# Kernel tuning notes

Hardware: AMD Instinct MI355X
Metric: run time of the kernel (lower is better)

## Reference

```python
import jax, jax.numpy as jnp
import numpy as np


def setup_inputs() -> dict:
    key = jax.random.key(0)
    k1, k2, k3, k4 = jax.random.split(key, 4)
    B, C, N, T = 16, 64, 2048, 24
    x = jax.random.normal(k1, (B, C, N, T), dtype=jnp.float32)
    adj = jax.random.uniform(k2, (N, N), dtype=jnp.float32)
    # Learned parameters (initialized to zeros in the original; random here
    # so the reference exercises nontrivial math).
    Gw = jax.random.normal(k3, (T, T), dtype=jnp.float32) * 0.1
    alpha = jax.random.normal(k4, (C,), dtype=jnp.float32) * 0.1
    return {"x": x, "adj": adj, "Gw": Gw, "alpha": alpha}


def reference(x, adj, Gw, alpha):
    # k = q = einsum('bcnt,c->bnt')  (channel-reduced features)
    k = jnp.einsum('bcnt,c->bnt', x, alpha)
    # scores[b,n,m] = k[b,n,:] @ Gw @ k[b,m,:]
    kG = jnp.einsum('bnt,ts->bns', k, Gw)          # [B,N,T]
    scores = jnp.einsum('bns,bms->bnm', kG, k)     # [B,N,N]
    att = jax.nn.softmax(scores, axis=-1)
    # adjacency-masked weighted aggregation over neighbors
    return jnp.einsum('bnm,bcmt->bcnt', att * adj, x)
```

## Files before the change

kernel.cpp:

```cpp
#include <hip/hip_runtime.h>
#include <hip/hip_bf16.h>

#define BB 16
#define CC 64
#define NN 2048
#define TT 24
#define JJ (CC*TT)
#define NT (NN*TT)

typedef unsigned short u16;
typedef unsigned int u32;
typedef __bf16 bf16x8 __attribute__((ext_vector_type(8)));
typedef u16 u16x8 __attribute__((ext_vector_type(8)));
typedef float f32x4 __attribute__((ext_vector_type(4)));
typedef u32 u32x4 __attribute__((ext_vector_type(4)));

static __device__ __forceinline__ u16 f2bf(float f) {
  union { float f; u32 u; } v; v.f = f;
  u32 u = v.u;
  u += 0x7fffu + ((u >> 16) & 1u);
  return (u16)(u >> 16);
}
static __device__ __forceinline__ float bf2f(u16 h) {
  union { u32 u; float f; } v; v.u = ((u32)h) << 16; return v.f;
}
static __device__ __forceinline__ bf16x8 ld_bf8(const u16* p) {
  return __builtin_bit_cast(bf16x8, *(const u16x8*)p);
}
#define MFMA16(a,b,c) __builtin_amdgcn_mfma_f32_16x16x32_bf16((a),(b),(c),0,0,0)

static __device__ __forceinline__ void gload16(const u16* g, u16* lds) {
  __builtin_amdgcn_global_load_lds(
      (const __attribute__((address_space(1))) u32*)g,
      (__attribute__((address_space(3))) u32*)lds, 16, 0, 0);
}
static __device__ __forceinline__ int SG(int r) { return (r ^ (r >> 2)) & 3; }

__global__ __launch_bounds__(256) void kA(
    const float* __restrict__ x, const float* __restrict__ alpha,
    u16* __restrict__ xT, float* __restrict__ kpart) {
  int bid = blockIdx.x;
  int b  = bid >> 5;
  int mt = (bid >> 1) & 15;
  int ch = bid & 1;
  int m0 = mt * 128;
  int tid = threadIdx.x;
  __shared__ float tile[128][25];
  float kacc[12];
  #pragma unroll
  for (int e = 0; e < 12; ++e) kacc[e] = 0.f;

  for (int c = ch*32; c < ch*32 + 32; ++c) {
    const float4* src4 = (const float4*)(x + ((size_t)(b*CC + c)*NN + m0)*TT);
    float a = alpha[c];
    float4 v[3];
    #pragma unroll
    for (int q = 0; q < 3; ++q) v[q] = src4[tid*3 + q];
    __syncthreads();
    #pragma unroll
    for (int q = 0; q < 3; ++q) {
      int idx = tid*3 + q;
      int mm = idx / 6, off = (idx - mm*6)*4;
      tile[mm][off]   = v[q].x; tile[mm][off+1] = v[q].y;
      tile[mm][off+2] = v[q].z; tile[mm][off+3] = v[q].w;
      kacc[q*4+0] += a*v[q].x; kacc[q*4+1] += a*v[q].y;
      kacc[q*4+2] += a*v[q].z; kacc[q*4+3] += a*v[q].w;
    }
    __syncthreads();
    #pragma unroll
    for (int qq = 0; qq < 6; ++qq) {
      int idx = tid*6 + qq;
      int t = idx >> 6, mp = idx & 63;
      u32 lo = f2bf(tile[2*mp][t]);
      u32 hi = f2bf(tile[2*mp+1][t]);
      ((u32*)(xT + ((size_t)((b*CC + c)*TT + t))*NN + m0))[mp] = lo | (hi << 16);
    }
  }
  float* kp = kpart + (size_t)ch*BB*NT + (size_t)b*NT + (size_t)m0*TT + tid*12;
  #pragma unroll
  for (int q = 0; q < 3; ++q)
    *(float4*)(kp + q*4) = make_float4(kacc[q*4], kacc[q*4+1], kacc[q*4+2], kacc[q*4+3]);
}

__global__ __launch_bounds__(256) void k2_prep(
    const float* __restrict__ kpart, const float* __restrict__ Gw,
    u16* __restrict__ kGhi, u16* __restrict__ kGlo,
    u16* __restrict__ kPhi, u16* __restrict__ kPlo) {
  __shared__ float gw[TT*TT];
  for (int i = threadIdx.x; i < TT*TT; i += 256) gw[i] = Gw[i];
  __syncthreads();
  int row = blockIdx.x * blockDim.x + threadIdx.x;
  if (row >= BB*NN) return;
  float kr[TT];
  const float4* s0 = (const float4*)(kpart + (size_t)row*TT);
  const float4* s1 = (const float4*)(kpart + (size_t)BB*NT + (size_t)row*TT);
  #pragma unroll
  for (int q = 0; q < 6; ++q) {
    float4 a = s0[q], bv = s1[q];
    kr[4*q]   = a.x + bv.x; kr[4*q+1] = a.y + bv.y;
    kr[4*q+2] = a.z + bv.z; kr[4*q+3] = a.w + bv.w;
  }
  float o[TT];
  #pragma unroll
  for (int s = 0; s < TT; ++s) o[s] = 0.f;
  #pragma unroll
  for (int t = 0; t < TT; ++t) {
    float kv = kr[t];
    #pragma unroll
    for (int s = 0; s < TT; ++s) o[s] += kv * gw[t*TT + s];
  }
  size_t rb = (size_t)row * 32;
  u32* ghi = (u32*)(kGhi + rb); u32* glo = (u32*)(kGlo + rb);
  u32* phi = (u32*)(kPhi + rb); u32* plo = (u32*)(kPlo + rb);
  #pragma unroll
  for (int sp = 0; sp < 16; ++sp) {
    float v0 = (2*sp   < TT) ? o[2*sp]   : 0.f;
    float v1 = (2*sp+1 < TT) ? o[2*sp+1] : 0.f;
    u16 h0 = f2bf(v0), h1 = f2bf(v1);
    u16 l0 = f2bf(v0 - bf2f(h0)), l1 = f2bf(v1 - bf2f(h1));
    ghi[sp] = (u32)h0 | ((u32)h1 << 16);
    glo[sp] = (u32)l0 | ((u32)l1 << 16);
    float w0 = (2*sp   < TT) ? kr[2*sp]   : 0.f;
    float w1 = (2*sp+1 < TT) ? kr[2*sp+1] : 0.f;
    u16 ph0 = f2bf(w0), ph1 = f2bf(w1);
    u16 pl0 = f2bf(w0 - bf2f(ph0)), pl1 = f2bf(w1 - bf2f(ph1));
    phi[sp] = (u32)ph0 | ((u32)ph1 << 16);
    plo[sp] = (u32)pl0 | ((u32)pl1 << 16);
  }
}

__global__ __launch_bounds__(256) void kW(
    const u16* __restrict__ kGhi, const u16* __restrict__ kGlo,
    const u16* __restrict__ kPhi, const u16* __restrict__ kPlo,
    const float* __restrict__ adj, u16* __restrict__ Wm,
    float* __restrict__ Zpart) {
  int bid = blockIdx.x;
  int b = bid >> 8, nt = (bid >> 4) & 15, mt = bid & 15;
  int tid = threadIdx.x;
  int w = tid >> 6, l = tid & 63;
  __shared__ u16 wlds[128][128];
  size_t kgb = ((size_t)b*NN + nt*128) * 32;
  bf16x8 ahi[2], alo[2];
  #pragma unroll
  for (int nf = 0; nf < 2; ++nf) {
    size_t off = kgb + (size_t)(w*32 + nf*16 + (l & 15))*32 + (l >> 4)*8;
    ahi[nf] = ld_bf8(kGhi + off);
    alo[nf] = ld_bf8(kGlo + off);
  }
  f32x4 acc[2][8];
  #pragma unroll
  for (int mf = 0; mf < 8; ++mf) {
    size_t off = ((size_t)b*NN + mt*128 + mf*16 + (l & 15))*32 + (l >> 4)*8;
    bf16x8 bhi = ld_bf8(kPhi + off);
    bf16x8 blo = ld_bf8(kPlo + off);
    #pragma unroll
    for (int nf = 0; nf < 2; ++nf) {
      f32x4 a = {0.f, 0.f, 0.f, 0.f};
      a = MFMA16(ahi[nf], blo, a);
      a = MFMA16(alo[nf], bhi, a);
      a = MFMA16(ahi[nf], bhi, a);
      acc[nf][mf] = a;
    }
  }
  #pragma unroll
  for (int nf = 0; nf < 2; ++nf)
    #pragma unroll
    for (int r = 0; r < 4; ++r) {
      int nl = w*32 + nf*16 + (l >> 4)*4 + r;
      float rs = 0.f;
      #pragma unroll
      for (int mf = 0; mf < 8; ++mf) {
        int ml = mf*16 + (l & 15);
        float e = __expf(acc[nf][mf][r]);
        rs += e;
        float wv = e * adj[(size_t)(nt*128 + nl)*NN + mt*128 + ml];
        wlds[nl][ml] = f2bf(wv);
      }
      #pragma unroll
      for (int st = 1; st < 16; st <<= 1) rs += __shfl_xor(rs, st);
      if ((l & 15) == 0)
        Zpart[((size_t)b*NN + nt*128 + nl)*16 + mt] = rs;
    }
  __syncthreads();
  int row = tid >> 1, half = tid & 1;
  const u32x4* s4 = (const u32x4*)&wlds[row][half*64];
  u32x4* d4 = (u32x4*)(Wm + ((size_t)(b*NN + nt*128 + row))*NN + mt*128 + half*64);
  #pragma unroll
  for (int q = 0; q < 8; ++q) d4[q] = s4[q];
}

__global__ __launch_bounds__(512, 2) void k4_gemm(
    const u16* __restrict__ Wm, const u16* __restrict__ xT,
    const float* __restrict__ Zpart, float* __restrict__ out) {
  __shared__ __align__(16) u16 sA[4*256*32];
  __shared__ __align__(16) u16 sB[4*256*32];
  __shared__ float rinv[256];

  int bid = blockIdx.x;
  int wg = (bid & 7) * 96 + (bid >> 3);
  int b = wg / 48; int rem = wg - b*48;
  int nt = rem / 6, jt = rem - nt*6;

  int tid = threadIdx.x;
  int w = tid >> 6, l = tid & 63;
  int wr = w >> 2, wc = w & 3;

  if (tid < 256) {
    const float* zp = Zpart + ((size_t)b*NN + nt*256 + tid)*16;
    float s = 0.f;
    #pragma unroll
    for (int i = 0; i < 16; ++i) s += zp[i];
    rinv[tid] = 1.f / s;
  }
  asm volatile("s_waitcnt vmcnt(0)" ::: "memory");

  int rs0 = w*32 + (l >> 2);
  int g0 = (l & 3) ^ SG(rs0);
  const u16* pA0 = Wm + ((size_t)b*NN + (size_t)(nt*256 + rs0))*NN + g0*8;
  const u16* pA1 = Wm + ((size_t)b*NN + (size_t)(nt*256 + rs0 + 16))*NN + g0*8;
  const u16* pB0 = xT + ((size_t)b*JJ + (size_t)(jt*256 + rs0))*NN + g0*8;
  const u16* pB1 = xT + ((size_t)b*JJ + (size_t)(jt*256 + rs0 + 16))*NN + g0*8;
  u16* dA0 = sA + (w*32)*32;
  u16* dA1 = sA + (w*32 + 16)*32;
  u16* dB0 = sB + (w*32)*32;
  u16* dB1 = sB + (w*32 + 16)*32;

  int rA = wr*128 + (l & 15);
  int baseA = rA*32 + (((l >> 4) ^ SG(rA)) << 3);
  int rB = wc*64 + (l & 15);
  int baseB = rB*32 + (((l >> 4) ^ SG(rB)) << 3);

  f32x4 acc[8][4];
  #pragma unroll
  for (int f = 0; f < 8; ++f)
    #pragma unroll
    for (int cf = 0; cf < 4; ++cf) acc[f][cf] = (f32x4){0.f,0.f,0.f,0.f};

  #pragma unroll
  for (int tt = 0; tt < 3; ++tt) {
    gload16(pA0, dA0 + tt*8192); pA0 += 32;
    gload16(pA1, dA1 + tt*8192); pA1 += 32;
    gload16(pB0, dB0 + tt*8192); pB0 += 32;
    gload16(pB1, dB1 + tt*8192); pB1 += 32;
  }
  asm volatile("s_waitcnt vmcnt(8)" ::: "memory");
  __builtin_amdgcn_s_barrier();
  asm volatile("" ::: "memory");

  for (int t = 0; t < 64; ++t) {
    int buf = t & 3;
    if (t < 61) {
      int sb = (t + 3) & 3;
      gload16(pA0, dA0 + sb*8192); pA0 += 32;
      gload16(pA1, dA1 + sb*8192); pA1 += 32;
      gload16(pB0, dB0 + sb*8192); pB0 += 32;
      gload16(pB1, dB1 + sb*8192); pB1 += 32;
    }
    const u16* sAb = sA + buf*8192 + baseA;
    const u16* sBb = sB + buf*8192 + baseB;
    bf16x8 af[8], bv[4];
    #pragma unroll
    for (int f = 0; f < 8; ++f) af[f] = ld_bf8(sAb + f*512);
    #pragma unroll
    for (int cf = 0; cf < 4; ++cf) bv[cf] = ld_bf8(sBb + cf*512);
    __builtin_amdgcn_s_setprio(1);
    #pragma unroll
    for (int f = 0; f < 8; ++f)
      #pragma unroll
      for (int cf = 0; cf < 4; ++cf)
        acc[f][cf] = MFMA16(af[f], bv[cf], acc[f][cf]);
    __builtin_amdgcn_s_setprio(0);
    if (t < 63) {
      if (t <= 60)      asm volatile("s_waitcnt vmcnt(8)" ::: "memory");
      else if (t == 61) asm volatile("s_waitcnt vmcnt(4)" ::: "memory");
      else              asm volatile("s_waitcnt vmcnt(0)" ::: "memory");
      __builtin_amdgcn_s_barrier();
      asm volatile("" ::: "memory");
    }
  }

  #pragma unroll
  for (int f = 0; f < 8; ++f)
    #pragma unroll
    for (int cf = 0; cf < 4; ++cf) {
      int j = jt*256 + wc*64 + cf*16 + (l & 15);
      int c = j / TT, t_ = j - c*TT;
      #pragma unroll
      for (int r = 0; r < 4; ++r) {
        int nl = wr*128 + f*16 + (l >> 4)*4 + r;
        out[((size_t)(b*CC + c)*NN + nt*256 + nl)*TT + t_] = acc[f][cf][r] * rinv[nl];
      }
    }
}

extern "C" void kernel_launch(void* const* d_in, const int* in_sizes, int n_in,
                              void* d_out, int out_size, void* d_ws, size_t ws_size,
                              hipStream_t stream) {
  const float* x     = (const float*)d_in[0];
  const float* adj   = (const float*)d_in[1];
  const float* Gw    = (const float*)d_in[2];
  const float* alpha = (const float*)d_in[3];
  float* out = (float*)d_out;

  const size_t XT_B = (size_t)BB*JJ*NN*2;
  const size_t W_B  = (size_t)BB*NN*NN*2;
  const size_t KS_B = (size_t)BB*NN*32*2;
  char* base = (char*)d_ws;
  u16*   xT    = (u16*)base;
  u16*   Wm    = (u16*)(base + XT_B);
  float* kpart = (float*)(base + XT_B);
  u16*   kGhi  = (u16*)(base + XT_B + W_B);
  u16*   kGlo  = (u16*)(base + XT_B + W_B + KS_B);
  u16*   kPhi  = (u16*)(base + XT_B + W_B + 2*KS_B);
  u16*   kPlo  = (u16*)(base + XT_B + W_B + 3*KS_B);
  float* Zpart = (float*)(base + XT_B + W_B + 4*KS_B);

  kA<<<512, 256, 0, stream>>>(x, alpha, xT, kpart);
  k2_prep<<<BB*NN/256, 256, 0, stream>>>(kpart, Gw, kGhi, kGlo, kPhi, kPlo);
  kW<<<BB*16*16, 256, 0, stream>>>(kGhi, kGlo, kPhi, kPlo, adj, Wm, Zpart);
  k4_gemm<<<768, 512, 0, stream>>>(Wm, xT, Zpart, out);
}
```

Baseline: 465.2 us.

## Restructure GEMM main loop to BK=64 double-buffered ping-pong with interleaved staging

Rewrites the k4_gemm main loop. It now uses K-tiles of 64 with two LDS buffers instead of four buffers of K=32. Each iteration is split into four MFMA phases, with LDS fragment loads and half-tile global-to-LDS loads interleaved between barriers, plus an 8-way XOR swizzle and setprio. The aim is to overlap memory traffic with MFMA work and halve the loop-trip overhead, at the cost of many more barriers per iteration and tighter vmcnt bookkeeping.

```diff
diff --git a/kernel.cpp b/kernel.cpp
--- a/kernel.cpp
+++ b/kernel.cpp
@@ -34,7 +34,6 @@
       (const __attribute__((address_space(1))) u32*)g,
       (__attribute__((address_space(3))) u32*)lds, 16, 0, 0);
 }
-static __device__ __forceinline__ int SG(int r) { return (r ^ (r >> 2)) & 3; }
 
 __global__ __launch_bounds__(256) void kA(
     const float* __restrict__ x, const float* __restrict__ alpha,
@@ -192,8 +191,8 @@
 __global__ __launch_bounds__(512, 2) void k4_gemm(
     const u16* __restrict__ Wm, const u16* __restrict__ xT,
     const float* __restrict__ Zpart, float* __restrict__ out) {
-  __shared__ __align__(16) u16 sA[4*256*32];
-  __shared__ __align__(16) u16 sB[4*256*32];
+  __shared__ __align__(16) u16 sA[2*2*128*64];
+  __shared__ __align__(16) u16 sB[2*2*128*64];
   __shared__ float rinv[256];
 
   int bid = blockIdx.x;
@@ -204,6 +203,127 @@
   int tid = threadIdx.x;
   int w = tid >> 6, l = tid & 63;
   int wr = w >> 2, wc = w & 3;
+  int l15 = l & 15, l4 = l >> 4, lx = l & 7;
+
+  int g0 = ((l4)     ^ lx) << 3;
+  int g1 = ((4 + l4) ^ lx) << 3;
+  int rbA = wr*8192 + l15*64;
+  int rbB = (wc>>1)*8192 + ((wc&1)*64 + l15)*64;
+
+  int srow = tid >> 3, sslot = tid & 7;
+  int sgx = (sslot ^ (srow & 7)) << 3;
+  const size_t ROW64 = (size_t)64 * NN;
+  const u16* pAlo = Wm + (size_t)b*NN*NN + (size_t)(nt*256 + srow)*NN + sgx;
+  const u16* pAhi = pAlo + (size_t)128*NN;
+  const u16* pBlo = xT + (size_t)b*JJ*NN + (size_t)(jt*256 + srow)*NN + sgx;
+  const u16* pBhi = pBlo + (size_t)128*NN;
+  int wbase = w << 9;
+
+#define STG(ptr, arr, dbuf, half) do { \
+    gload16(ptr, arr + ((dbuf)<<14) + ((half)<<13) + wbase); \
+    gload16(ptr + ROW64, arr + ((dbuf)<<14) + ((half)<<13) + 4096 + wbase); \
+    ptr += 64; } while (0)
+
+  f32x4 acc[8][4];
+  #pragma unroll
+  for (int f = 0; f < 8; ++f)
+    #pragma unroll
+    for (int cf = 0; cf < 4; ++cf) acc[f][cf] = (f32x4){0.f,0.f,0.f,0.f};
+  bf16x8 a[4][2], bv[4][2];
+
+  STG(pBlo, sB, 0, 0); STG(pBhi, sB, 0, 1);
+  STG(pAlo, sA, 0, 0); STG(pAhi, sA, 0, 1);
+  STG(pBlo, sB, 1, 0); STG(pBhi, sB, 1, 1);
+  asm volatile("s_waitcnt vmcnt(4)" ::: "memory");
+  __builtin_amdgcn_sched_barrier(0);
+  __builtin_amdgcn_s_barrier();
+
+  for (int kt = 0; kt < 32; ++kt) {
+    int p = kt & 1, q = p ^ 1;
+    int pb = p << 14;
+    #pragma unroll
+    for (int f = 0; f < 4; ++f) {
+      a[f][0] = ld_bf8(sA + pb + rbA + f*1024 + g0);
+      a[f][1] = ld_bf8(sA + pb + rbA + f*1024 + g1);
+    }
+    #pragma unroll
+    for (int cf = 0; cf < 2; ++cf) {
+      bv[cf][0] = ld_bf8(sB + pb + rbB + cf*1024 + g0);
+      bv[cf][1] = ld_bf8(sB + pb + rbB + cf*1024 + g1);
+    }
+    if (kt < 31) STG(pAlo, sA, q, 0);
+    __builtin_amdgcn_s_barrier();
+    asm volatile("s_waitcnt lgkmcnt(0)" ::: "memory");
+    __builtin_amdgcn_sched_barrier(0);
+    __builtin_amdgcn_s_setprio(1);
+    #pragma unroll
+    for (int f = 0; f < 4; ++f)
+      #pragma unroll
+      for (int cf = 0; cf < 2; ++cf) {
+        acc[f][cf] = MFMA16(a[f][0], bv[cf][0], acc[f][cf]);
+        acc[f][cf] = MFMA16(a[f][1], bv[cf][1], acc[f][cf]);
+      }
+    __builtin_amdgcn_s_setprio(0);
+    __builtin_amdgcn_s_barrier();
+    #pragma unroll
+    for (int cf = 2; cf < 4; ++cf) {
+      bv[cf][0] = ld_bf8(sB + pb + rbB + cf*1024 + g0);
+      bv[cf][1] = ld_bf8(sB + pb + rbB + cf*1024 + g1);
+    }
+    if (kt < 31) STG(pAhi, sA, q, 1);
+    __builtin_amdgcn_s_barrier();
+    asm volatile("s_waitcnt lgkmcnt(0)" ::: "memory");
+    __builtin_amdgcn_sched_barrier(0);
+    __builtin_amdgcn_s_setprio(1);
+    #pragma unroll
+    for (int f = 0; f < 4; ++f)
+      #pragma unroll
+      for (int cf = 2; cf < 4; ++cf) {
+        acc[f][cf] = MFMA16(a[f][0], bv[cf][0], acc[f][cf]);
+        acc[f][cf] = MFMA16(a[f][1], bv[cf][1], acc[f][cf]);
+      }
+    __builtin_amdgcn_s_setprio(0);
+    __builtin_amdgcn_s_barrier();
+    #pragma unroll
+    for (int f = 0; f < 4; ++f) {
+      a[f][0] = ld_bf8(sA + pb + rbA + (f+4)*1024 + g0);
+      a[f][1] = ld_bf8(sA + pb + rbA + (f+4)*1024 + g1);
+    }
+    if (kt < 30) STG(pBlo, sB, p, 0);
+    __builtin_amdgcn_s_barrier();
+    asm volatile("s_waitcnt lgkmcnt(0)" ::: "memory");
+    __builtin_amdgcn_sched_barrier(0);
+    __builtin_amdgcn_s_setprio(1);
+    #pragma unroll
+    for (int f = 0; f < 4; ++f)
+      #pragma unroll
+      for (int cf = 0; cf < 2; ++cf) {
+        acc[f+4][cf] = MFMA16(a[f][0], bv[cf][0], acc[f+4][cf]);
+        acc[f+4][cf] = MFMA16(a[f][1], bv[cf][1], acc[f+4][cf]);
+      }
+    __builtin_amdgcn_s_setprio(0);
+    __builtin_amdgcn_s_barrier();
+    if (kt < 30) STG(pBhi, sB, p, 1);
+    __builtin_amdgcn_s_barrier();
+    __builtin_amdgcn_s_setprio(1);
+    #pragma unroll
+    for (int f = 0; f < 4; ++f)
+      #pragma unroll
+      for (int cf = 2; cf < 4; ++cf) {
+        acc[f+4][cf] = MFMA16(a[f][0], bv[cf][0], acc[f+4][cf]);
+        acc[f+4][cf] = MFMA16(a[f][1], bv[cf][1], acc[f+4][cf]);
+      }
+    __builtin_amdgcn_s_setprio(0);
+    if (kt < 30) {
+      asm volatile("s_waitcnt vmcnt(4)" ::: "memory");
+      __builtin_amdgcn_sched_barrier(0);
+    } else if (kt == 30) {
+      asm volatile("s_waitcnt vmcnt(0)" ::: "memory");
+      __builtin_amdgcn_sched_barrier(0);
+    }
+    __builtin_amdgcn_s_barrier();
+  }
+#undef STG
 
   if (tid < 256) {
     const float* zp = Zpart + ((size_t)b*NN + nt*256 + tid)*16;
@@ -212,82 +332,17 @@
     for (int i = 0; i < 16; ++i) s += zp[i];
     rinv[tid] = 1.f / s;
   }
-  asm volatile("s_waitcnt vmcnt(0)" ::: "memory");
-
-  int rs0 = w*32 + (l >> 2);
-  int g0 = (l & 3) ^ SG(rs0);
-  const u16* pA0 = Wm + ((size_t)b*NN + (size_t)(nt*256 + rs0))*NN + g0*8;
-  const u16* pA1 = Wm + ((size_t)b*NN + (size_t)(nt*256 + rs0 + 16))*NN + g0*8;
-  const u16* pB0 = xT + ((size_t)b*JJ + (size_t)(jt*256 + rs0))*NN + g0*8;
-  const u16* pB1 = xT + ((size_t)b*JJ + (size_t)(jt*256 + rs0 + 16))*NN + g0*8;
-  u16* dA0 = sA + (w*32)*32;
-  u16* dA1 = sA + (w*32 + 16)*32;
-  u16* dB0 = sB + (w*32)*32;
-  u16* dB1 = sB + (w*32 + 16)*32;
-
-  int rA = wr*128 + (l & 15);
-  int baseA = rA*32 + (((l >> 4) ^ SG(rA)) << 3);
-  int rB = wc*64 + (l & 15);
-  int baseB = rB*32 + (((l >> 4) ^ SG(rB)) << 3);
-
-  f32x4 acc[8][4];
+  __syncthreads();
+
   #pragma unroll
   for (int f = 0; f < 8; ++f)
     #pragma unroll
-    for (int cf = 0; cf < 4; ++cf) acc[f][cf] = (f32x4){0.f,0.f,0.f,0.f};
-
-  #pragma unroll
-  for (int tt = 0; tt < 3; ++tt) {
-    gload16(pA0, dA0 + tt*8192); pA0 += 32;
-    gload16(pA1, dA1 + tt*8192); pA1 += 32;
-    gload16(pB0, dB0 + tt*8192); pB0 += 32;
-    gload16(pB1, dB1 + tt*8192); pB1 += 32;
-  }
-  asm volatile("s_waitcnt vmcnt(8)" ::: "memory");
-  __builtin_amdgcn_s_barrier();
-  asm volatile("" ::: "memory");
-
-  for (int t = 0; t < 64; ++t) {
-    int buf = t & 3;
-    if (t < 61) {
-      int sb = (t + 3) & 3;
-      gload16(pA0, dA0 + sb*8192); pA0 += 32;
-      gload16(pA1, dA1 + sb*8192); pA1 += 32;
-      gload16(pB0, dB0 + sb*8192); pB0 += 32;
-      gload16(pB1, dB1 + sb*8192); pB1 += 32;
-    }
-    const u16* sAb = sA + buf*8192 + baseA;
-    const u16* sBb = sB + buf*8192 + baseB;
-    bf16x8 af[8], bv[4];
-    #pragma unroll
-    for (int f = 0; f < 8; ++f) af[f] = ld_bf8(sAb + f*512);
-    #pragma unroll
-    for (int cf = 0; cf < 4; ++cf) bv[cf] = ld_bf8(sBb + cf*512);
-    __builtin_amdgcn_s_setprio(1);
-    #pragma unroll
-    for (int f = 0; f < 8; ++f)
-      #pragma unroll
-      for (int cf = 0; cf < 4; ++cf)
-        acc[f][cf] = MFMA16(af[f], bv[cf], acc[f][cf]);
-    __builtin_amdgcn_s_setprio(0);
-    if (t < 63) {
-      if (t <= 60)      asm volatile("s_waitcnt vmcnt(8)" ::: "memory");
-      else if (t == 61) asm volatile("s_waitcnt vmcnt(4)" ::: "memory");
-      else              asm volatile("s_waitcnt vmcnt(0)" ::: "memory");
-      __builtin_amdgcn_s_barrier();
-      asm volatile("" ::: "memory");
-    }
-  }
-
-  #pragma unroll
-  for (int f = 0; f < 8; ++f)
-    #pragma unroll
     for (int cf = 0; cf < 4; ++cf) {
-      int j = jt*256 + wc*64 + cf*16 + (l & 15);
+      int j = jt*256 + wc*64 + cf*16 + l15;
       int c = j / TT, t_ = j - c*TT;
       #pragma unroll
       for (int r = 0; r < 4; ++r) {
-        int nl = wr*128 + f*16 + (l >> 4)*4 + r;
+        int nl = wr*128 + f*16 + l4*4 + r;
         out[((size_t)(b*CC + c)*NN + nt*256 + nl)*TT + t_] = acc[f][cf][r] * rinv[nl];
       }
     }
```

Measured after the change: 422.5 us. -9.2%, faster.
